# Optimization experiments

Measured on AMD Instinct MI355X. Metric: run time of the kernel, lower is better.

## Reference

```python
import jax, jax.numpy as jnp
import numpy as np

NEG_SLOPE = 0.2  # PyG GATv2Conv default negative_slope


def gatv2(x, edge_index, w_l, w_r, att, bias):
    # x: [G, N, F]  (G = batch*step independent graphs sharing edge_index)
    G, N, F = x.shape
    H, C = att.shape
    # add self loops (PyG default add_self_loops=True)
    loops = jnp.arange(N, dtype=edge_index.dtype)
    src = jnp.concatenate([edge_index[0], loops])  # [E]
    dst = jnp.concatenate([edge_index[1], loops])  # [E]
    # linear projections for source / target nodes
    x_l = (x @ w_l).reshape(G, N, H, C)  # source projection
    x_r = (x @ w_r).reshape(G, N, H, C)  # target projection
    # gather along edges -> [E, G, H, C] (edge axis leading for segment ops)
    src_f = jnp.take(x_l, src, axis=1).transpose(1, 0, 2, 3)
    dst_f = jnp.take(x_r, dst, axis=1).transpose(1, 0, 2, 3)
    # GATv2 attention logit: a^T leaky_relu(W_l x_j + W_r x_i)
    e = jax.nn.leaky_relu(src_f + dst_f, NEG_SLOPE)
    logit = jnp.einsum('eghc,hc->egh', e, att)  # [E, G, H]
    # numerically-stable segment softmax over incoming edges per dst node
    m = jax.ops.segment_max(logit, dst, num_segments=N)  # [N, G, H]
    ex = jnp.exp(logit - m[dst])
    denom = jax.ops.segment_sum(ex, dst, num_segments=N)  # [N, G, H]
    alpha = ex / denom[dst]  # [E, G, H]
    # weighted scatter-add aggregation
    out = jax.ops.segment_sum(alpha[..., None] * src_f, dst, num_segments=N)  # [N,G,H,C]
    out = out.transpose(1, 0, 2, 3).reshape(G, N, H * C) + bias
    return out


def setup_inputs() -> dict:
    key = jax.random.key(0)
    ks = jax.random.split(key, 6)
    B, T, N, F = 8, 10, 1000, 64
    E, H, C = 8000, 1, 64
    x = jax.random.normal(ks[0], (B, T, N, F), dtype=jnp.float32)
    edge_index = jax.random.randint(ks[1], (2, E), 0, N, dtype=jnp.int64)
    s = 1.0 / np.sqrt(F)
    w_l = jax.random.normal(ks[2], (F, H * C), dtype=jnp.float32) * s
    w_r = jax.random.normal(ks[3], (F, H * C), dtype=jnp.float32) * s
    att = jax.random.normal(ks[4], (H, C), dtype=jnp.float32) * (1.0 / np.sqrt(C))
    bias = jnp.zeros((H * C,), dtype=jnp.float32)
    return {"x": x, "edge_index": edge_index, "w_l": w_l, "w_r": w_r, "att": att, "bias": bias}


def reference(x, edge_index, w_l, w_r, att, bias):
    B, T, N, F = x.shape
    out = gatv2(x.reshape(B * T, N, F), edge_index, w_l, w_r, att, bias)
    return out.reshape(B, T, N, -1)
```

## Files before the change

### kernel.cpp

```cpp
#include <hip/hip_runtime.h>
#include <hip/hip_bf16.h>


#define GG 80
#define NN 1000
#define EE 8000
#define MM 80000
#define PAD 40
#define NEG_SLOPE 0.2f

typedef __attribute__((ext_vector_type(8))) short short8;
typedef __attribute__((ext_vector_type(4))) float floatx4;

__device__ __forceinline__ unsigned short f2b(float f) {
    unsigned int u = __float_as_uint(f);
    unsigned int r = u + 0x7fffu + ((u >> 16) & 1u);
    return (unsigned short)(r >> 16);
}

__global__ __launch_bounds__(256) void proj_csr_kernel(
    const float* __restrict__ x,
    const float* __restrict__ wl,
    const float* __restrict__ wr,
    const int* __restrict__ ei32,
    unsigned short* __restrict__ XLt,
    unsigned short* __restrict__ XRt,
    int* __restrict__ list2)
{
    __shared__ __align__(16) unsigned short Wt[128 * 72];
    __shared__ int cnt[1024];
    const int t = threadIdx.x;

    if (blockIdx.x == 313) {
        int oddw = ei32[2 * t + 1];
        const int stride = __any(oddw != 0) ? 1 : 2;

        for (int i = t; i < 1024; i += 256) cnt[i] = 0;
        __syncthreads();

        int dv[32], sv[32];
#pragma unroll
        for (int k = 0; k < 32; k++) {
            int e = t + (k << 8);
            dv[k] = (e < EE) ? ei32[(size_t)(EE + e) * stride] : -1;
        }
#pragma unroll
        for (int k = 0; k < 32; k++) {
            int e = t + (k << 8);
            sv[k] = (e < EE) ? ei32[(size_t)e * stride] : 0;
        }
#pragma unroll
        for (int k = 0; k < 32; k++) {
            if (dv[k] >= 0) {
                int pos = atomicAdd(&cnt[dv[k]], 1);
                if (pos < PAD - 2) list2[dv[k] * PAD + 1 + pos] = sv[k];
            }
        }
        __syncthreads();
        for (int n = t; n < NN; n += 256) {
            int c = min(cnt[n], PAD - 2);
            list2[n * PAD + 1 + c] = n;
            list2[n * PAD] = c + 1;
        }
        return;
    }

    for (int idx = t; idx < 8192; idx += 256) {
        int half = idx >> 12;
        int k = (idx & 4095) >> 6;
        int c = idx & 63;
        float v = half ? wr[k * 64 + c] : wl[k * 64 + c];
        Wt[(c + half * 64) * 72 + k] = f2b(v);
    }
    __syncthreads();

    const int wave = t >> 6;
    const int lane = t & 63;
    const int quad = lane >> 4;
    const int lm   = lane & 15;
    const int Rb   = (blockIdx.x * 4 + wave) * 64;

    short8 Bf[2][8];
#pragma unroll
    for (int ks = 0; ks < 2; ks++)
#pragma unroll
        for (int sub = 0; sub < 8; sub++)
            Bf[ks][sub] = *(const short8*)(&Wt[(sub * 16 + lm) * 72 + ks * 32 + quad * 8]);

    const float4* x4 = (const float4*)x;

#pragma unroll
    for (int sm = 0; sm < 4; sm++) {
        const int rbase = Rb + sm * 16;
        const int r  = rbase + lm;
        const int rc = (r < MM) ? r : (MM - 1);

        short8 Af[2];
#pragma unroll
        for (int ks = 0; ks < 2; ks++) {
            float4 p = x4[(size_t)rc * 16 + ks * 8 + quad * 2];
            float4 q = x4[(size_t)rc * 16 + ks * 8 + quad * 2 + 1];
            short8 a;
            a[0] = (short)f2b(p.x); a[1] = (short)f2b(p.y);
            a[2] = (short)f2b(p.z); a[3] = (short)f2b(p.w);
            a[4] = (short)f2b(q.x); a[5] = (short)f2b(q.y);
            a[6] = (short)f2b(q.z); a[7] = (short)f2b(q.w);
            Af[ks] = a;
        }

        floatx4 acc[8];
#pragma unroll
        for (int sub = 0; sub < 8; sub++) acc[sub] = (floatx4)(0.f);
#pragma unroll
        for (int ks = 0; ks < 2; ks++)
#pragma unroll
            for (int sub = 0; sub < 8; sub++)
                acc[sub] = __builtin_amdgcn_mfma_f32_16x16x32_bf16(Af[ks], Bf[ks][sub], acc[sub], 0, 0, 0);

#pragma unroll
        for (int reg = 0; reg < 4; reg++) {
            int rr = rbase + quad * 4 + reg;
            if (rr < MM) {
                int g = rr / 1000;
                int n = rr - g * 1000;
                size_t ob = ((size_t)n * GG + g) * 64 + lm;
#pragma unroll
                for (int sub = 0; sub < 4; sub++)
                    XLt[ob + sub * 16] = f2b(acc[sub][reg]);
#pragma unroll
                for (int sub = 4; sub < 8; sub++)
                    XRt[ob + (sub - 4) * 16] = f2b(acc[sub][reg]);
            }
        }
    }
}

__global__ __launch_bounds__(128) void agg_kernel(
    const unsigned short* __restrict__ XLt,
    const unsigned short* __restrict__ XRt,
    const int* __restrict__ list2,
    const float* __restrict__ att,
    const float* __restrict__ bias,
    float* __restrict__ out)
{
    const int t = threadIdx.x;
    const int d = blockIdx.x;
    const int g = blockIdx.y * 16 + (t >> 3);
    const int cg = t & 7;

    const int* hdr = list2 + d * PAD;
    const int cnt = __builtin_amdgcn_readfirstlane(hdr[0]);

    float xr[8], a6[8], a4[8], bv[8];
    {
        const uint4 u = *(const uint4*)(XRt + ((size_t)d * GG + g) * 64 + cg * 8);
        const unsigned int uw[4] = {u.x, u.y, u.z, u.w};
#pragma unroll
        for (int q = 0; q < 4; q++) {
            xr[2 * q + 0] = __uint_as_float(uw[q] << 16);
            xr[2 * q + 1] = __uint_as_float(uw[q] & 0xffff0000u);
        }
        const float4 a0 = *(const float4*)(att + cg * 8);
        const float4 a1 = *(const float4*)(att + cg * 8 + 4);
        const float4 b0 = *(const float4*)(bias + cg * 8);
        const float4 b1 = *(const float4*)(bias + cg * 8 + 4);
        const float aa[8] = {a0.x, a0.y, a0.z, a0.w, a1.x, a1.y, a1.z, a1.w};
        const float bb[8] = {b0.x, b0.y, b0.z, b0.w, b1.x, b1.y, b1.z, b1.w};
#pragma unroll
        for (int j = 0; j < 8; j++) {
            a6[j] = 0.6f * aa[j];
            a4[j] = 0.4f * aa[j];
            bv[j] = bb[j];
        }
    }

    float acc[8];
#pragma unroll
    for (int j = 0; j < 8; j++) acc[j] = 0.f;
    float dn = 0.f;

    for (int i = 0; i < cnt; i += 16) {
        uint4 u[16];
#pragma unroll
        for (int c = 0; c < 4; c++) {
            if (i + 4 * c < cnt) {
#pragma unroll
                for (int e2 = 0; e2 < 4; e2++) {
                    const int idx = i + 4 * c + e2;
                    const int s = hdr[1 + ((idx < cnt) ? idx : 0)];
                    u[4 * c + e2] = *(const uint4*)(XLt + ((size_t)s * GG + g) * 64 + cg * 8);
                }
            }
        }
#pragma unroll
        for (int c = 0; c < 4; c++) {
            if (i + 4 * c < cnt) {
#pragma unroll
                for (int e2 = 0; e2 < 4; e2++) {
                    const int e = 4 * c + e2;
                    const unsigned int uw[4] = {u[e].x, u[e].y, u[e].z, u[e].w};
                    float xf[8];
#pragma unroll
                    for (int q = 0; q < 4; q++) {
                        xf[2 * q]     = __uint_as_float(uw[q] << 16);
                        xf[2 * q + 1] = __uint_as_float(uw[q] & 0xffff0000u);
                    }
                    float p = 0.f;
#pragma unroll
                    for (int j = 0; j < 8; j++) {
                        const float v = xf[j] + xr[j];
                        p = fmaf(a6[j], v, p);
                        p = fmaf(a4[j], fabsf(v), p);
                    }
                    p += __shfl_xor(p, 1, 64);
                    p += __shfl_xor(p, 2, 64);
                    p += __shfl_xor(p, 4, 64);
                    const float w = (i + e < cnt) ? __expf(p) : 0.f;
                    dn += w;
#pragma unroll
                    for (int j = 0; j < 8; j++) acc[j] = fmaf(w, xf[j], acc[j]);
                }
            }
        }
    }

    const float inv = 1.f / dn;
    float4 r0, r1;
    r0.x = acc[0] * inv + bv[0];
    r0.y = acc[1] * inv + bv[1];
    r0.z = acc[2] * inv + bv[2];
    r0.w = acc[3] * inv + bv[3];
    r1.x = acc[4] * inv + bv[4];
    r1.y = acc[5] * inv + bv[5];
    r1.z = acc[6] * inv + bv[6];
    r1.w = acc[7] * inv + bv[7];
    float* po = out + ((size_t)g * NN + d) * 64 + cg * 8;
    *(float4*)po = r0;
    *(float4*)(po + 4) = r1;
}

extern "C" void kernel_launch(void* const* d_in, const int* in_sizes, int n_in,
                              void* d_out, int out_size, void* d_ws, size_t ws_size,
                              hipStream_t stream) {
    const float* x    = (const float*)d_in[0];
    const int*   ei   = (const int*)d_in[1];
    const float* wl   = (const float*)d_in[2];
    const float* wr   = (const float*)d_in[3];
    const float* att  = (const float*)d_in[4];
    const float* bias = (const float*)d_in[5];
    float* out = (float*)d_out;

    char* ws = (char*)d_ws;
    int* list2 = (int*)ws;
    unsigned short* XLt = (unsigned short*)(ws + 262144);
    unsigned short* XRt = XLt + (size_t)NN * GG * 64;

    hipLaunchKernelGGL(proj_csr_kernel, dim3(314), dim3(256), 0, stream,
                       x, wl, wr, ei, XLt, XRt, list2);
    hipLaunchKernelGGL(agg_kernel, dim3(NN, 5), dim3(128), 0, stream,
                       XLt, XRt, list2, att, bias, out);
}
```

Baseline: 106.6 us.

## Precompute linear part of leaky-relu attention logit per node in projection

Splits leaky_relu(v) into 0.6*v + 0.4*|v|. The linear 0.6*att·(xl+xr) term becomes a per-node scalar pair (SL6, SR6), computed in the projection kernel's epilogue with a shuffle reduction. The aggregation kernel then does only the |v| FMA per channel and adds two scalars, which removes one FMA per element in the hot loop. The cost is an extra scalar gather per edge and extra writes and shuffles in the projection kernel.

```diff
diff --git a/kernel.cpp b/kernel.cpp
--- a/kernel.cpp
+++ b/kernel.cpp
@@ -23,8 +23,11 @@
     const float* __restrict__ wl,
     const float* __restrict__ wr,
     const int* __restrict__ ei32,
+    const float* __restrict__ att,
     unsigned short* __restrict__ XLt,
     unsigned short* __restrict__ XRt,
+    float* __restrict__ SL6,
+    float* __restrict__ SR6,
     int* __restrict__ list2)
 {
     __shared__ __align__(16) unsigned short Wt[128 * 72];
@@ -86,6 +89,10 @@
 #pragma unroll
         for (int sub = 0; sub < 8; sub++)
             Bf[ks][sub] = *(const short8*)(&Wt[(sub * 16 + lm) * 72 + ks * 32 + quad * 8]);
+
+    float a_s[4];
+#pragma unroll
+    for (int sub = 0; sub < 4; sub++) a_s[sub] = 0.6f * att[sub * 16 + lm];
 
     const float4* x4 = (const float4*)x;
 
@@ -124,12 +131,28 @@
                 int g = rr / 1000;
                 int n = rr - g * 1000;
                 size_t ob = ((size_t)n * GG + g) * 64 + lm;
-#pragma unroll
-                for (int sub = 0; sub < 4; sub++)
-                    XLt[ob + sub * 16] = f2b(acc[sub][reg]);
-#pragma unroll
-                for (int sub = 4; sub < 8; sub++)
-                    XRt[ob + (sub - 4) * 16] = f2b(acc[sub][reg]);
+                float pl = 0.f, pr = 0.f;
+#pragma unroll
+                for (int sub = 0; sub < 4; sub++) {
+                    unsigned short b = f2b(acc[sub][reg]);
+                    XLt[ob + sub * 16] = b;
+                    pl = fmaf(a_s[sub], __uint_as_float((unsigned int)b << 16), pl);
+                }
+#pragma unroll
+                for (int sub = 4; sub < 8; sub++) {
+                    unsigned short b = f2b(acc[sub][reg]);
+                    XRt[ob + (sub - 4) * 16] = b;
+                    pr = fmaf(a_s[sub - 4], __uint_as_float((unsigned int)b << 16), pr);
+                }
+#pragma unroll
+                for (int m = 1; m < 16; m <<= 1) {
+                    pl += __shfl_xor(pl, m, 64);
+                    pr += __shfl_xor(pr, m, 64);
+                }
+                if (lm == 0) {
+                    SL6[(size_t)n * GG + g] = pl;
+                    SR6[(size_t)n * GG + g] = pr;
+                }
             }
         }
     }
@@ -141,6 +164,8 @@
     const int* __restrict__ list2,
     const float* __restrict__ att,
     const float* __restrict__ bias,
+    const float* __restrict__ SL6,
+    const float* __restrict__ SR6,
     float* __restrict__ out)
 {
     const int t = threadIdx.x;
@@ -151,7 +176,7 @@
     const int* hdr = list2 + d * PAD;
     const int cnt = __builtin_amdgcn_readfirstlane(hdr[0]);
 
-    float xr[8], a6[8], a4[8], bv[8];
+    float xr[8], a4[8];
     {
         const uint4 u = *(const uint4*)(XRt + ((size_t)d * GG + g) * 64 + cg * 8);
         const unsigned int uw[4] = {u.x, u.y, u.z, u.w};
@@ -162,17 +187,11 @@
         }
         const float4 a0 = *(const float4*)(att + cg * 8);
         const float4 a1 = *(const float4*)(att + cg * 8 + 4);
-        const float4 b0 = *(const float4*)(bias + cg * 8);
-        const float4 b1 = *(const float4*)(bias + cg * 8 + 4);
         const float aa[8] = {a0.x, a0.y, a0.z, a0.w, a1.x, a1.y, a1.z, a1.w};
-        const float bb[8] = {b0.x, b0.y, b0.z, b0.w, b1.x, b1.y, b1.z, b1.w};
-#pragma unroll
-        for (int j = 0; j < 8; j++) {
-            a6[j] = 0.6f * aa[j];
-            a4[j] = 0.4f * aa[j];
-            bv[j] = bb[j];
-        }
-    }
+#pragma unroll
+        for (int j = 0; j < 8; j++) a4[j] = 0.4f * aa[j];
+    }
+    const float sr6 = SR6[(size_t)d * GG + g];
 
     float acc[8];
 #pragma unroll
@@ -181,23 +200,25 @@
 
     for (int i = 0; i < cnt; i += 16) {
         uint4 u[16];
-#pragma unroll
-        for (int c = 0; c < 4; c++) {
-            if (i + 4 * c < cnt) {
-#pragma unroll
-                for (int e2 = 0; e2 < 4; e2++) {
-                    const int idx = i + 4 * c + e2;
+        float sl[16];
+#pragma unroll
+        for (int c = 0; c < 8; c++) {
+            if (i + 2 * c < cnt) {
+#pragma unroll
+                for (int e2 = 0; e2 < 2; e2++) {
+                    const int idx = i + 2 * c + e2;
                     const int s = hdr[1 + ((idx < cnt) ? idx : 0)];
-                    u[4 * c + e2] = *(const uint4*)(XLt + ((size_t)s * GG + g) * 64 + cg * 8);
-                }
-            }
-        }
-#pragma unroll
-        for (int c = 0; c < 4; c++) {
-            if (i + 4 * c < cnt) {
-#pragma unroll
-                for (int e2 = 0; e2 < 4; e2++) {
-                    const int e = 4 * c + e2;
+                    u[2 * c + e2] = *(const uint4*)(XLt + ((size_t)s * GG + g) * 64 + cg * 8);
+                    sl[2 * c + e2] = SL6[(size_t)s * GG + g];
+                }
+            }
+        }
+#pragma unroll
+        for (int c = 0; c < 8; c++) {
+            if (i + 2 * c < cnt) {
+#pragma unroll
+                for (int e2 = 0; e2 < 2; e2++) {
+                    const int e = 2 * c + e2;
                     const unsigned int uw[4] = {u[e].x, u[e].y, u[e].z, u[e].w};
                     float xf[8];
 #pragma unroll
@@ -209,12 +230,12 @@
 #pragma unroll
                     for (int j = 0; j < 8; j++) {
                         const float v = xf[j] + xr[j];
-                        p = fmaf(a6[j], v, p);
                         p = fmaf(a4[j], fabsf(v), p);
                     }
                     p += __shfl_xor(p, 1, 64);
                     p += __shfl_xor(p, 2, 64);
                     p += __shfl_xor(p, 4, 64);
+                    p += sl[e] + sr6;
                     const float w = (i + e < cnt) ? __expf(p) : 0.f;
                     dn += w;
 #pragma unroll
@@ -225,15 +246,17 @@
     }
 
     const float inv = 1.f / dn;
+    const float4 b0 = *(const float4*)(bias + cg * 8);
+    const float4 b1 = *(const float4*)(bias + cg * 8 + 4);
     float4 r0, r1;
-    r0.x = acc[0] * inv + bv[0];
-    r0.y = acc[1] * inv + bv[1];
-    r0.z = acc[2] * inv + bv[2];
-    r0.w = acc[3] * inv + bv[3];
-    r1.x = acc[4] * inv + bv[4];
-    r1.y = acc[5] * inv + bv[5];
-    r1.z = acc[6] * inv + bv[6];
-    r1.w = acc[7] * inv + bv[7];
+    r0.x = fmaf(acc[0], inv, b0.x);
+    r0.y = fmaf(acc[1], inv, b0.y);
+    r0.z = fmaf(acc[2], inv, b0.z);
+    r0.w = fmaf(acc[3], inv, b0.w);
+    r1.x = fmaf(acc[4], inv, b1.x);
+    r1.y = fmaf(acc[5], inv, b1.y);
+    r1.z = fmaf(acc[6], inv, b1.z);
+    r1.w = fmaf(acc[7], inv, b1.w);
     float* po = out + ((size_t)g * NN + d) * 64 + cg * 8;
     *(float4*)po = r0;
     *(float4*)(po + 4) = r1;
@@ -254,9 +277,11 @@
     int* list2 = (int*)ws;
     unsigned short* XLt = (unsigned short*)(ws + 262144);
     unsigned short* XRt = XLt + (size_t)NN * GG * 64;
+    float* SL6 = (float*)(ws + 262144 + 2 * (size_t)NN * GG * 64 * 2);
+    float* SR6 = SL6 + (size_t)NN * GG;
 
     hipLaunchKernelGGL(proj_csr_kernel, dim3(314), dim3(256), 0, stream,
-                       x, wl, wr, ei, XLt, XRt, list2);
+                       x, wl, wr, ei, att, XLt, XRt, SL6, SR6, list2);
     hipLaunchKernelGGL(agg_kernel, dim3(NN, 5), dim3(128), 0, stream,
-                       XLt, XRt, list2, att, bias, out);
-}
+                       XLt, XRt, list2, att, bias, SL6, SR6, out);
+}
```

Measured after the change: 109.4 us. 2.6% more time.
